# Optimization experiments

Hardware: AMD Instinct MI355X
Metric: run time of the kernel (lower is better)

The kernel has to match this reference:

```python
import jax, jax.numpy as jnp
import numpy as np

B, S, D = 128, 256, 768          # batch, seq (pre-sentinel), encoder dim
ARC, TAG = 500, 100              # arc / tag representation dims
LAYERS, TOPK = 2, 8              # config['gnn_layers'], config['top_k']
SP = S + 1                       # seq_len after head sentinel


def setup_inputs() -> dict:
    key = jax.random.key(0)
    ks = jax.random.split(key, 32)
    sc = 0.02
    inp = {
        'inputs': jax.random.normal(ks[0], (B, S, D), jnp.float32),
        'tag_embeddings': jax.random.randint(ks[1], (B, S), 0, 50),
        'mask': jnp.ones((B, S), jnp.int32),
        'head_indices': jax.random.randint(ks[2], (B, S), 0, S),
        'head_tags': jax.random.randint(ks[3], (B, S), 0, 50),
        # parameters
        'head_sentinel': jax.random.normal(ks[4], (D,), jnp.float32),
        'W_ha': jax.random.normal(ks[5], (D, ARC)) * sc, 'b_ha': jnp.zeros((ARC,)),
        'W_da': jax.random.normal(ks[6], (D, ARC)) * sc, 'b_da': jnp.zeros((ARC,)),
        'W_ht': jax.random.normal(ks[7], (D, TAG)) * sc, 'b_ht': jnp.zeros((TAG,)),
        'W_dt': jax.random.normal(ks[8], (D, TAG)) * sc, 'b_dt': jnp.zeros((TAG,)),
        # bilinear attention: use_input_biases=True -> (ARC+1, ARC+1), plus scalar bias
        'bil_W': jax.random.normal(ks[9], (LAYERS + 1, ARC + 1, ARC + 1)) * sc,
        'bil_b': jnp.zeros((LAYERS + 1,)),
        # GCNConv params (PyG: x @ W, symmetric-normalized aggregate, + bias)
        'c1a_W': jax.random.normal(ks[10], (ARC, ARC)) * sc, 'c1a_b': jnp.zeros((ARC,)),
        'c2a_W': jax.random.normal(ks[11], (ARC, ARC)) * sc, 'c2a_b': jnp.zeros((ARC,)),
        'c1r_W': jax.random.normal(ks[12], (TAG, TAG)) * sc, 'c1r_b': jnp.zeros((TAG,)),
        'c2r_W': jax.random.normal(ks[13], (TAG, TAG)) * sc, 'c2r_b': jnp.zeros((TAG,)),
    }
    return inp


def bilinear_attn(m1, m2, W, b):
    # AllenNLP BilinearMatrixAttention with use_input_biases=True
    ones1 = jnp.ones(m1.shape[:-1] + (1,), m1.dtype)
    m1b = jnp.concatenate([m1, ones1], -1)
    m2b = jnp.concatenate([m2, ones1], -1)
    return jnp.einsum('bie,ef,bjf->bij', m1b, W, m2b) + b


def batch_top_k(probs, k):
    # probs: [B, SP, SP] row-softmaxed; edge j(head)->i(dep) for each row's top-k cols,
    # with global (batched) node indexing.
    vals, idx = jax.lax.top_k(probs, k)                      # [B, SP, k]
    offs = (jnp.arange(B) * SP)[:, None, None]
    src = (idx + offs).reshape(-1)
    dst = (jnp.broadcast_to(jnp.arange(SP)[None, :, None], idx.shape) + offs).reshape(-1)
    return src, dst, vals.reshape(-1)


def gcn_conv(x, src, dst, ew, W, b):
    # PyG GCNConv: x@W, add self-loops (weight 1), sym norm, scatter-add at dst, + bias
    N = x.shape[0]
    x = x @ W
    loop = jnp.arange(N)
    row = jnp.concatenate([src, loop])
    col = jnp.concatenate([dst, loop])
    w = jnp.concatenate([ew, jnp.ones((N,), x.dtype)])
    deg = jax.ops.segment_sum(w, col, num_segments=N)
    dinv = jnp.where(deg > 0, jax.lax.rsqrt(deg), 0.0)
    norm = dinv[row] * w * dinv[col]
    out = jax.ops.segment_sum(x[row] * norm[:, None], col, num_segments=N)
    return out + b


def reference(inputs, tag_embeddings, mask, head_indices, head_tags,
              head_sentinel, W_ha, b_ha, W_da, b_da, W_ht, b_ht, W_dt, b_dt,
              bil_W, bil_b, c1a_W, c1a_b, c2a_W, c2a_b, c1r_W, c1r_b, c2r_W, c2r_b):
    elu = jax.nn.elu
    x = jnp.concatenate([jnp.broadcast_to(head_sentinel, (B, 1, D)), inputs], axis=1)  # [B,SP,D]
    head_arc = elu(x @ W_ha + b_ha)
    dept_arc = elu(x @ W_da + b_da)
    head_tag = elu(x @ W_ht + b_ht)
    dep_tag = elu(x @ W_dt + b_dt)

    def two_conv(feat, W1, b1, W2, b2, src, dst, ew):
        h = gcn_conv(feat.reshape(B * SP, -1), src, dst, ew, W1, b1)
        h = gcn_conv(elu(h), src, dst, ew, W2, b2)
        return h.reshape(B, SP, -1)

    for k in range(LAYERS):
        arc_logits = bilinear_attn(head_arc, dept_arc, bil_W[k], bil_b[k])
        arc_probs = jax.nn.softmax(arc_logits, axis=-1)
        src, dst, ew = batch_top_k(arc_probs, TOPK)
        head_arc = two_conv(head_arc, c1a_W, c1a_b, c2a_W, c2a_b, src, dst, ew)
        dept_arc = two_conv(dept_arc, c1a_W, c1a_b, c2a_W, c2a_b, src, dst, ew)
        head_tag = two_conv(head_tag, c1r_W, c1r_b, c2r_W, c2r_b, src, dst, ew)
        dep_tag = two_conv(dep_tag, c1r_W, c1r_b, c2r_W, c2r_b, src, dst, ew)

    arc_logits = bilinear_attn(head_arc, dept_arc, bil_W[-1], bil_b[-1])
    return arc_logits, head_tag, dep_tag
```

## Files before the change

kernel.cpp:

```cpp
#include <hip/hip_runtime.h>
#include <hip/hip_bf16.h>
#include <math.h>
#include <cstddef>

namespace {

constexpr int kB   = 128;
constexpr int kS   = 256;
constexpr int kD   = 768;
constexpr int kSP  = 257;
constexpr int kN   = kB * kSP;
constexpr int kARC = 500;
constexpr int kTAG = 100;
constexpr int KA   = 512;
constexpr int KT   = 128;

typedef __attribute__((ext_vector_type(8))) short short8;
typedef __attribute__((ext_vector_type(4))) float floatx4;
typedef __attribute__((ext_vector_type(2))) float floatx2;
typedef __attribute__((ext_vector_type(4))) unsigned short ushort4v;
typedef __attribute__((ext_vector_type(2))) unsigned short ushort2v;
typedef __hip_bfloat16 bf;

__device__ __forceinline__ float bfval(bf h) { return __bfloat162float(h); }
__device__ __forceinline__ unsigned short bfbits(bf h) {
  unsigned short u; __builtin_memcpy(&u, &h, 2); return u;
}
__device__ __forceinline__ void splitf(float x, bf* h, bf* l) {
  bf hh = __float2bfloat16(x);
  *h = hh;
  *l = __float2bfloat16(x - __bfloat162float(hh));
}

__device__ __forceinline__ void gload16(const bf* g, bf* l) {
  __builtin_amdgcn_global_load_lds(
      (const __attribute__((address_space(1))) void*)g,
      (__attribute__((address_space(3))) void*)l, 16, 0, 0);
}

__global__ void detect_dtype_n(const unsigned* __restrict__ raw, int* __restrict__ flag,
                               int nwords) {
  int lane = threadIdx.x;
  int ok = 0, nz = 0;
  if (lane < nwords) {
    unsigned w = raw[lane];
    if (w != 0u) {
      nz = 1;
      int e = (w >> 7) & 0xFF;
      ok = (e >= 90 && e <= 140);
    }
  }
  unsigned long long ball_ok = __ballot(ok);
  unsigned long long ball_nz = __ballot(nz);
  if (lane == 0) {
    int cok = __popcll(ball_ok), cnz = __popcll(ball_nz);
    flag[0] = (cok * 4 >= cnz * 3) ? 1 : 0;
  }
}

__device__ __forceinline__ float rawload(const void* p, size_t i, int bfm) {
  return bfm ? __bfloat162float(((const bf*)p)[i]) : ((const float*)p)[i];
}

__global__ void conv_off(const void* __restrict__ src, float* __restrict__ dst,
                         int n, long off, const int* __restrict__ flag) {
  int i = blockIdx.x * 256 + threadIdx.x;
  if (i >= n) return;
  dst[i] = rawload(src, (size_t)off + i, *flag);
}

__global__ void wsplit_t(const void* __restrict__ src, const int* __restrict__ flag,
                         long srcOff, int ldsrc, int K, int N, int Kpad,
                         bf* __restrict__ Wh, bf* __restrict__ Wl) {
  long idx = (long)blockIdx.x * 256 + threadIdx.x;
  if (idx >= (long)N * Kpad) return;
  int n = (int)(idx / Kpad), k = (int)(idx % Kpad);
  float v = (k < K) ? rawload(src, (size_t)srcOff + (size_t)k * ldsrc + n, *flag) : 0.f;
  bf h, l;
  splitf(v, &h, &l);
  Wh[idx] = h; Wl[idx] = l;
}

__global__ void xsplit(const void* __restrict__ inp, const void* __restrict__ sent,
                       const int* __restrict__ fi, const int* __restrict__ fs,
                       bf* __restrict__ xh, bf* __restrict__ xl, int g0, int NG) {
  long idx = (long)blockIdx.x * 256 + threadIdx.x;
  long tot = (long)NG * (kD / 4);
  if (idx >= tot) return;
  int n = (int)(idx / (kD / 4));
  int k = (int)(idx % (kD / 4)) * 4;
  int b = n / kSP, r = n - b * kSP;
  const void* src;
  size_t base;
  int bfm;
  if (r == 0) { src = sent; base = (size_t)k; bfm = *fs; }
  else {
    src = inp;
    base = ((size_t)((g0 + b) * kS + (r - 1))) * kD + k;
    bfm = *fi;
  }
  float v[4];
  if (bfm) {
    ushort4v s = *(const ushort4v*)((const unsigned short*)src + base);
#pragma unroll
    for (int j = 0; j < 4; ++j) {
      bf h; unsigned short u = s[j];
      __builtin_memcpy(&h, &u, 2);
      v[j] = __bfloat162float(h);
    }
  } else {
    floatx4 f4 = *(const floatx4*)((const float*)src + base);
#pragma unroll
    for (int j = 0; j < 4; ++j) v[j] = f4[j];
  }
  ushort4v h4, l4;
#pragma unroll
  for (int j = 0; j < 4; ++j) {
    bf h, l;
    splitf(v[j], &h, &l);
    h4[j] = bfbits(h); l4[j] = bfbits(l);
  }
  size_t o = (size_t)n * kD + k;
  *(ushort4v*)((unsigned short*)xh + o) = h4;
  *(ushort4v*)((unsigned short*)xl + o) = l4;
}

constexpr int BM = 128, BN = 128, BK = 32;

template <int EPI, int OUTF32>
__global__ __launch_bounds__(256) void gemm_sp(
    const bf* __restrict__ Ah, const bf* __restrict__ Al, int lda,
    const bf* __restrict__ Bh, const bf* __restrict__ Bl, int ldb,
    bf* __restrict__ Ch, bf* __restrict__ Cl, float* __restrict__ Cf, int ldc,
    int M, int N, int K, const float* __restrict__ bias) {
  __shared__ bf sAh[2][BM][BK];
  __shared__ bf sAl[2][BM][BK];
  __shared__ bf sBh[2][BN][BK];
  __shared__ bf sBl[2][BN][BK];
  const int tid = threadIdx.x;
  const int lane = tid & 63, wave = tid >> 6;
  const int quad = lane >> 4, l15 = lane & 15;
  const int wm = (wave >> 1) * 64, wn = (wave & 1) * 64;
  const int m0 = blockIdx.x * BM, n0 = blockIdx.y * BN;
  const int lrow = lane >> 2, lkof = (lane & 3) * 8;

  const bf *pAh[2], *pAl[2], *pBh[2], *pBl[2];
  int rb[2];
#pragma unroll
  for (int jj = 0; jj < 2; ++jj) {
    rb[jj] = wave * 32 + jj * 16;
    int gm = m0 + rb[jj] + lrow; if (gm > M - 1) gm = M - 1;
    int gn = n0 + rb[jj] + lrow; if (gn > N - 1) gn = N - 1;
    pAh[jj] = Ah + (size_t)gm * lda + lkof;
    pAl[jj] = Al + (size_t)gm * lda + lkof;
    pBh[jj] = Bh + (size_t)gn * ldb + lkof;
    pBl[jj] = Bl + (size_t)gn * ldb + lkof;
  }

  auto stage = [&](int bi, int k0) {
#pragma unroll
    for (int jj = 0; jj < 2; ++jj) {
      gload16(pAh[jj] + k0, &sAh[bi][rb[jj]][0]);
      gload16(pAl[jj] + k0, &sAl[bi][rb[jj]][0]);
      gload16(pBh[jj] + k0, &sBh[bi][rb[jj]][0]);
      gload16(pBl[jj] + k0, &sBl[bi][rb[jj]][0]);
    }
  };

  floatx4 acc[4][4] = {};
  stage(0, 0);
  int cur = 0;
  for (int k0 = 0; k0 < K; k0 += BK) {
    __syncthreads();
    if (k0 + BK < K) stage(cur ^ 1, k0 + BK);
    short8 a_h[4], a_l[4], b_h[4], b_l[4];
#pragma unroll
    for (int t = 0; t < 4; ++t) {
      a_h[t] = *(const short8*)&sAh[cur][wm + t * 16 + l15][quad * 8];
      a_l[t] = *(const short8*)&sAl[cur][wm + t * 16 + l15][quad * 8];
      b_h[t] = *(const short8*)&sBh[cur][wn + t * 16 + l15][quad * 8];
      b_l[t] = *(const short8*)&sBl[cur][wn + t * 16 + l15][quad * 8];
    }
#pragma unroll
    for (int mt = 0; mt < 4; ++mt)
#pragma unroll
      for (int nt = 0; nt < 4; ++nt) {
        acc[mt][nt] = __builtin_amdgcn_mfma_f32_16x16x32_bf16(a_h[mt], b_h[nt], acc[mt][nt], 0, 0, 0);
        acc[mt][nt] = __builtin_amdgcn_mfma_f32_16x16x32_bf16(a_h[mt], b_l[nt], acc[mt][nt], 0, 0, 0);
        acc[mt][nt] = __builtin_amdgcn_mfma_f32_16x16x32_bf16(a_l[mt], b_h[nt], acc[mt][nt], 0, 0, 0);
      }
    cur ^= 1;
  }
#pragma unroll
  for (int mt = 0; mt < 4; ++mt)
#pragma unroll
    for (int reg = 0; reg < 4; ++reg) {
      int m = m0 + wm + mt * 16 + quad * 4 + reg;
      if (m >= M) continue;
#pragma unroll
      for (int nt = 0; nt < 4; ++nt) {
        int n = n0 + wn + nt * 16 + l15;
        if (OUTF32) {
          if (n < N) {
            float v = acc[mt][nt][reg];
            if (EPI >= 1) v += bias[n];
            if (EPI == 1) v = v > 0.f ? v : expm1f(v);
            Cf[(size_t)m * ldc + n] = v;
          }
        } else {
          size_t o = (size_t)m * ldc + n;
          if (n < N) {
            float v = acc[mt][nt][reg];
            if (EPI >= 1) v += bias[n];
            if (EPI == 1) v = v > 0.f ? v : expm1f(v);
            bf h, l;
            splitf(v, &h, &l);
            Ch[o] = h; Cl[o] = l;
          } else if (n < ldc) {
            Ch[o] = __float2bfloat16(0.f);
            Cl[o] = __float2bfloat16(0.f);
          }
        }
      }
    }
}

__global__ __launch_bounds__(256) void bilnt_sp(
    const bf* __restrict__ Th, const bf* __restrict__ Tl,
    const bf* __restrict__ Fh, const bf* __restrict__ Fl,
    float* __restrict__ out, const float* __restrict__ bilb, int bidx,
    int g0, int globOut) {
  __shared__ bf sAh[2][BM][BK];
  __shared__ bf sAl[2][BM][BK];
  __shared__ bf sBh[2][BN][BK];
  __shared__ bf sBl[2][BN][BK];
  const int z = blockIdx.z;
  const int tid = threadIdx.x;
  const int lane = tid & 63, wave = tid >> 6;
  const int quad = lane >> 4, l15 = lane & 15;
  const int wm = (wave >> 1) * 64, wn = (wave & 1) * 64;
  const int m0 = blockIdx.x * BM, n0 = blockIdx.y * BN;
  const int lrow = lane >> 2, lkof = (lane & 3) * 8;
  const bf* Ah = Th + (size_t)z * kSP * KA;
  const bf* Al = Tl + (size_t)z * kSP * KA;
  const bf* Bh = Fh + (size_t)z * kSP * KA;
  const bf* Bl = Fl + (size_t)z * kSP * KA;

  const bf *pAh[2], *pAl[2], *pBh[2], *pBl[2];
  int rb[2];
#pragma unroll
  for (int jj = 0; jj < 2; ++jj) {
    rb[jj] = wave * 32 + jj * 16;
    int gm = m0 + rb[jj] + lrow; if (gm > kSP - 1) gm = kSP - 1;
    int gn = n0 + rb[jj] + lrow; if (gn > kSP - 1) gn = kSP - 1;
    pAh[jj] = Ah + (size_t)gm * KA + lkof;
    pAl[jj] = Al + (size_t)gm * KA + lkof;
    pBh[jj] = Bh + (size_t)gn * KA + lkof;
    pBl[jj] = Bl + (size_t)gn * KA + lkof;
  }

  auto stage = [&](int bi, int k0) {
#pragma unroll
    for (int jj = 0; jj < 2; ++jj) {
      gload16(pAh[jj] + k0, &sAh[bi][rb[jj]][0]);
      gload16(pAl[jj] + k0, &sAl[bi][rb[jj]][0]);
      gload16(pBh[jj] + k0, &sBh[bi][rb[jj]][0]);
      gload16(pBl[jj] + k0, &sBl[bi][rb[jj]][0]);
    }
  };

  floatx4 acc[4][4] = {};
  stage(0, 0);
  int cur = 0;
  for (int k0 = 0; k0 < KA; k0 += BK) {
    __syncthreads();
    if (k0 + BK < KA) stage(cur ^ 1, k0 + BK);
    short8 a_h[4], a_l[4], b_h[4], b_l[4];
#pragma unroll
    for (int t = 0; t < 4; ++t) {
      a_h[t] = *(const short8*)&sAh[cur][wm + t * 16 + l15][quad * 8];
      a_l[t] = *(const short8*)&sAl[cur][wm + t * 16 + l15][quad * 8];
      b_h[t] = *(const short8*)&sBh[cur][wn + t * 16 + l15][quad * 8];
      b_l[t] = *(const short8*)&sBl[cur][wn + t * 16 + l15][quad * 8];
    }
#pragma unroll
    for (int mt = 0; mt < 4; ++mt)
#pragma unroll
      for (int nt = 0; nt < 4; ++nt) {
        acc[mt][nt] = __builtin_amdgcn_mfma_f32_16x16x32_bf16(a_h[mt], b_h[nt], acc[mt][nt], 0, 0, 0);
        acc[mt][nt] = __builtin_amdgcn_mfma_f32_16x16x32_bf16(a_h[mt], b_l[nt], acc[mt][nt], 0, 0, 0);
        acc[mt][nt] = __builtin_amdgcn_mfma_f32_16x16x32_bf16(a_l[mt], b_h[nt], acc[mt][nt], 0, 0, 0);
      }
    cur ^= 1;
  }
  const float sb = bilb[bidx];
  const int bb = globOut ? (g0 + z) : z;
#pragma unroll
  for (int mt = 0; mt < 4; ++mt)
#pragma unroll
    for (int reg = 0; reg < 4; ++reg) {
      int i = m0 + wm + mt * 16 + quad * 4 + reg;
      if (i >= kSP) continue;
      float rowterm = bfval(Ah[(size_t)i * KA + 500]) + bfval(Al[(size_t)i * KA + 500]) + sb;
#pragma unroll
      for (int nt = 0; nt < 4; ++nt) {
        int j = n0 + wn + nt * 16 + l15;
        if (j >= kSP) continue;
        out[((size_t)bb * kSP + i) * kSP + j] = acc[mt][nt][reg] + rowterm;
      }
    }
}

__global__ void softmax_topk(const float* __restrict__ logits,
                             int* __restrict__ idx8,
                             float* __restrict__ val8,
                             float* __restrict__ dinv) {
  const int row = blockIdx.x;
  const int lane = threadIdx.x;
  const int rowbase = row - (row % kSP);
  const float* L = logits + (size_t)row * kSP;
  float v[5];
  int c[5];
#pragma unroll
  for (int q = 0; q < 5; ++q) {
    int j = lane + q * 64;
    c[q] = j;
    v[q] = (j < kSP) ? L[j] : -INFINITY;
  }
  float m = v[0];
#pragma unroll
  for (int q = 1; q < 5; ++q) m = fmaxf(m, v[q]);
  for (int off = 32; off > 0; off >>= 1) m = fmaxf(m, __shfl_xor(m, off));
  float s = 0.f;
#pragma unroll
  for (int q = 0; q < 5; ++q) s += expf(v[q] - m);
  for (int off = 32; off > 0; off >>= 1) s += __shfl_xor(s, off);
  const float invs = 1.f / s;
  float degsum = 0.f;
  for (int t = 0; t < 8; ++t) {
    float bvv = -INFINITY;
    int bii = kSP;
#pragma unroll
    for (int q = 0; q < 5; ++q)
      if (v[q] > bvv) { bvv = v[q]; bii = c[q]; }
    for (int off = 32; off > 0; off >>= 1) {
      float ov = __shfl_xor(bvv, off);
      int oi = __shfl_xor(bii, off);
      if (ov > bvv || (ov == bvv && oi < bii)) { bvv = ov; bii = oi; }
    }
    float p = expf(bvv - m) * invs;
    degsum += p;
    if (lane == 0) { idx8[row * 8 + t] = rowbase + bii; val8[row * 8 + t] = p; }
#pragma unroll
    for (int q = 0; q < 5; ++q)
      if (c[q] == bii) v[q] = -INFINITY;
  }
  if (lane == 0) dinv[row] = 1.f / sqrtf(1.f + degsum);
}

template <int ELU, int OUTF32>
__global__ void gcn_agg(const float* __restrict__ Y, int ldy, int F,
                        const int* __restrict__ idx8, const float* __restrict__ val8,
                        const float* __restrict__ dinv, const float* __restrict__ bias,
                        bf* __restrict__ Zh, bf* __restrict__ Zl,
                        float* __restrict__ Zf, int ldzf) {
  const int n = blockIdx.x;
  __shared__ float w[9];
  __shared__ int srcs[8];
  const int t = threadIdx.x;
  if (t < 8) {
    int s = idx8[n * 8 + t];
    srcs[t] = s;
    w[t] = dinv[n] * val8[n * 8 + t] * dinv[s];
  } else if (t == 8) {
    float di = dinv[n];
    w[8] = di * di;
  }
  __syncthreads();
  const int lim = OUTF32 ? F : ldy;
  for (int f = t * 2; f < lim; f += (int)blockDim.x * 2) {
    size_t on = (size_t)n * ldy + f;
    if (!OUTF32 && f >= F) {
      ushort2v zz = {0, 0};
      *(ushort2v*)((unsigned short*)Zh + on) = zz;
      *(ushort2v*)((unsigned short*)Zl + on) = zz;
      continue;
    }
    floatx2 y0 = *(const floatx2*)(Y + on);
    float a0 = w[8] * y0[0], a1 = w[8] * y0[1];
#pragma unroll
    for (int e = 0; e < 8; ++e) {
      floatx2 ys = *(const floatx2*)(Y + (size_t)srcs[e] * ldy + f);
      a0 += w[e] * ys[0];
      a1 += w[e] * ys[1];
    }
    a0 += bias[f];
    a1 += bias[f + 1];
    if (ELU) {
      a0 = a0 > 0.f ? a0 : expm1f(a0);
      a1 = a1 > 0.f ? a1 : expm1f(a1);
    }
    if (OUTF32) {
      floatx2 o = {a0, a1};
      *(floatx2*)(Zf + (size_t)n * ldzf + f) = o;
    } else {
      bf h0, l0, h1, l1;
      splitf(a0, &h0, &l0);
      splitf(a1, &h1, &l1);
      ushort2v hv = {bfbits(h0), bfbits(h1)};
      ushort2v lv = {bfbits(l0), bfbits(l1)};
      *(ushort2v*)((unsigned short*)Zh + on) = hv;
      *(ushort2v*)((unsigned short*)Zl + on) = lv;
    }
  }
}

}

extern "C" void kernel_launch(void* const* d_in, const int* in_sizes, int n_in,
                              void* d_out, int out_size, void* d_ws, size_t ws_size,
                              hipStream_t stream) {
  (void)out_size;

  const int roleSize[20] = {kB * kS * kD, kD,
                            kD * kARC, kARC, kD * kARC, kARC,
                            kD * kTAG, kTAG, kD * kTAG, kTAG,
                            3 * 501 * 501, 3,
                            kARC * kARC, kARC, kARC * kARC, kARC,
                            kTAG * kTAG, kTAG, kTAG * kTAG, kTAG};
  const int roleOcc[20]  = {0, 0, 0, 0, 1, 1, 0, 0, 1, 1, 0, 0,
                            0, 2, 1, 3, 0, 2, 1, 3};
  int roleIdx[20] = {0, 5, 6, 7, 8, 9, 10, 11, 12, 13, 14, 15,
                     16, 17, 18, 19, 20, 21, 22, 23};
  for (int r = 0; r < 20; ++r) {
    int occ = 0, found = -1;
    for (int i = 0; i < n_in; ++i) {
      if (in_sizes[i] == roleSize[r]) {
        if (occ == roleOcc[r]) { found = i; break; }
        ++occ;
      }
    }
    if (found >= 0) roleIdx[r] = found;
    else if (roleIdx[r] >= n_in) roleIdx[r] = 0;
  }
  const void* src_of[20];
  for (int r = 0; r < 20; ++r) src_of[r] = d_in[roleIdx[r]];

  auto need_bytes = [](int GB) -> size_t {
    size_t NG = (size_t)GB * kSP, s = 0;
    auto al = [&](size_t b) { s += (b + 255) & ~(size_t)255; };
    al(256);
    for (int i = 0; i < 4; ++i) al((size_t)kARC * kD * 2);
    for (int i = 0; i < 4; ++i) al((size_t)kTAG * kD * 2);
    al(kARC * 4); al(kARC * 4); al(kTAG * 4); al(kTAG * 4);
    for (int i = 0; i < 6; ++i) al((size_t)501 * KA * 2);
    al(3 * 501 * 4); al(256);
    for (int i = 0; i < 4; ++i) al((size_t)kARC * KA * 2);
    for (int i = 0; i < 4; ++i) al((size_t)kTAG * KT * 2);
    al(kARC * 4); al(kARC * 4); al(kTAG * 4); al(kTAG * 4);
    al(NG * kD * 2); al(NG * kD * 2);
    for (int i = 0; i < 4; ++i) al(NG * KA * 2);
    for (int i = 0; i < 4; ++i) al(NG * KT * 2);
    al(NG * KA * 2); al(NG * KA * 2);
    al(NG * KA * 4);
    al(NG * kSP * 4);
    al(NG * 8 * 4); al(NG * 8 * 4); al(NG * 4);
    return s;
  };
  int GB = 1;
  for (int cand : {128, 64, 32, 16, 8, 4, 2, 1})
    if (need_bytes(cand) <= ws_size) { GB = cand; break; }
  const int G = kB / GB;
  const int NG = GB * kSP;
  const int mb = (NG + BM - 1) / BM;

  char* ws = (char*)d_ws;
  size_t off = 0;
  auto alloc = [&](size_t bytes) -> void* {
    void* p = ws + off;
    off += (bytes + 255) & ~(size_t)255;
    return p;
  };
  int* flags = (int*)alloc(256);
  bf *WtHAh = (bf*)alloc((size_t)kARC * kD * 2), *WtHAl = (bf*)alloc((size_t)kARC * kD * 2);
  bf *WtDAh = (bf*)alloc((size_t)kARC * kD * 2), *WtDAl = (bf*)alloc((size_t)kARC * kD * 2);
  bf *WtHTh = (bf*)alloc((size_t)kTAG * kD * 2), *WtHTl = (bf*)alloc((size_t)kTAG * kD * 2);
  bf *WtDTh = (bf*)alloc((size_t)kTAG * kD * 2), *WtDTl = (bf*)alloc((size_t)kTAG * kD * 2);
  float* bha = (float*)alloc(kARC * 4);
  float* bda = (float*)alloc(kARC * 4);
  float* bht = (float*)alloc(kTAG * 4);
  float* bdt = (float*)alloc(kTAG * 4);
  bf* bilWh[3]; bf* bilWl[3];
  for (int k = 0; k < 3; ++k) {
    bilWh[k] = (bf*)alloc((size_t)501 * KA * 2);
    bilWl[k] = (bf*)alloc((size_t)501 * KA * 2);
  }
  float* brow = (float*)alloc(3 * 501 * 4);
  float* bilbf = (float*)alloc(256);
  bf *c1ah = (bf*)alloc((size_t)kARC * KA * 2), *c1al = (bf*)alloc((size_t)kARC * KA * 2);
  bf *c2ah = (bf*)alloc((size_t)kARC * KA * 2), *c2al = (bf*)alloc((size_t)kARC * KA * 2);
  bf *c1rh = (bf*)alloc((size_t)kTAG * KT * 2), *c1rl = (bf*)alloc((size_t)kTAG * KT * 2);
  bf *c2rh = (bf*)alloc((size_t)kTAG * KT * 2), *c2rl = (bf*)alloc((size_t)kTAG * KT * 2);
  float* c1ab = (float*)alloc(kARC * 4);
  float* c2ab = (float*)alloc(kARC * 4);
  float* c1rb = (float*)alloc(kTAG * 4);
  float* c2rb = (float*)alloc(kTAG * 4);
  bf *xh = (bf*)alloc((size_t)NG * kD * 2), *xl = (bf*)alloc((size_t)NG * kD * 2);
  bf *fHAh = (bf*)alloc((size_t)NG * KA * 2), *fHAl = (bf*)alloc((size_t)NG * KA * 2);
  bf *fDAh = (bf*)alloc((size_t)NG * KA * 2), *fDAl = (bf*)alloc((size_t)NG * KA * 2);
  bf *fHTh = (bf*)alloc((size_t)NG * KT * 2), *fHTl = (bf*)alloc((size_t)NG * KT * 2);
  bf *fDTh = (bf*)alloc((size_t)NG * KT * 2), *fDTl = (bf*)alloc((size_t)NG * KT * 2);
  bf *Yh = (bf*)alloc((size_t)NG * KA * 2), *Yl = (bf*)alloc((size_t)NG * KA * 2);
  float* Yf = (float*)alloc((size_t)NG * KA * 4);
  float* logits = (float*)alloc((size_t)NG * kSP * 4);
  int*   idx8 = (int*)alloc((size_t)NG * 8 * 4);
  float* val8 = (float*)alloc((size_t)NG * 8 * 4);
  float* dinv = (float*)alloc((size_t)NG * 4);

  for (int r = 0; r < 20; ++r) {
    int n = roleSize[r];
    int nwords = n / 4; if (nwords < 1) nwords = 1; if (nwords > 64) nwords = 64;
    detect_dtype_n<<<1, 64, 0, stream>>>((const unsigned*)src_of[r], flags + r, nwords);
  }
  auto cvt = [&](int role, float* dst, int n, long o) {
    conv_off<<<(n + 255) / 256, 256, 0, stream>>>(src_of[role], dst, n, o, flags + role);
  };
  cvt(3, bha, kARC, 0); cvt(5, bda, kARC, 0); cvt(7, bht, kTAG, 0); cvt(9, bdt, kTAG, 0);
  cvt(11, bilbf, 3, 0);
  cvt(13, c1ab, kARC, 0); cvt(15, c2ab, kARC, 0); cvt(17, c1rb, kTAG, 0); cvt(19, c2rb, kTAG, 0);
  auto wsp = [&](int role, long o, int ldsrc, int K, int N, int Kpad, bf* Wh, bf* Wl) {
    long tot = (long)N * Kpad;
    wsplit_t<<<(int)((tot + 255) / 256), 256, 0, stream>>>(src_of[role], flags + role, o,
                                                           ldsrc, K, N, Kpad, Wh, Wl);
  };
  wsp(2, 0, kARC, kD, kARC, kD, WtHAh, WtHAl);
  wsp(4, 0, kARC, kD, kARC, kD, WtDAh, WtDAl);
  wsp(6, 0, kTAG, kD, kTAG, kD, WtHTh, WtHTl);
  wsp(8, 0, kTAG, kD, kTAG, kD, WtDTh, WtDTl);
  for (int k = 0; k < 3; ++k) {
    wsp(10, (long)k * 501 * 501, 501, 500, 501, KA, bilWh[k], bilWl[k]);
    cvt(10, brow + k * 501, 501, (long)k * 501 * 501 + 500 * 501);
  }
  wsp(12, 0, kARC, kARC, kARC, KA, c1ah, c1al);
  wsp(14, 0, kARC, kARC, kARC, KA, c2ah, c2al);
  wsp(16, 0, kTAG, kTAG, kTAG, KT, c1rh, c1rl);
  wsp(18, 0, kTAG, kTAG, kTAG, KT, c2rh, c2rl);

  float* outp = (float*)d_out;
  const size_t arc_elems = (size_t)kB * kSP * kSP;

  for (int g = 0; g < G; ++g) {
    const int g0 = g * GB;

    {
      long tot = (long)NG * (kD / 4);
      xsplit<<<(int)((tot + 255) / 256), 256, 0, stream>>>(
          src_of[0], src_of[1], flags + 0, flags + 1, xh, xl, g0, NG);
    }
    gemm_sp<1, 0><<<dim3(mb, 4), 256, 0, stream>>>(xh, xl, kD, WtHAh, WtHAl, kD,
                                                   fHAh, fHAl, nullptr, KA, NG, kARC, kD, bha);
    gemm_sp<1, 0><<<dim3(mb, 4), 256, 0, stream>>>(xh, xl, kD, WtDAh, WtDAl, kD,
                                                   fDAh, fDAl, nullptr, KA, NG, kARC, kD, bda);
    gemm_sp<1, 0><<<dim3(mb, 1), 256, 0, stream>>>(xh, xl, kD, WtHTh, WtHTl, kD,
                                                   fHTh, fHTl, nullptr, KT, NG, kTAG, kD, bht);
    gemm_sp<1, 0><<<dim3(mb, 1), 256, 0, stream>>>(xh, xl, kD, WtDTh, WtDTl, kD,
                                                   fDTh, fDTl, nullptr, KT, NG, kTAG, kD, bdt);

    for (int k = 0; k < 2; ++k) {
      gemm_sp<2, 0><<<dim3(mb, 4), 256, 0, stream>>>(fHAh, fHAl, KA, bilWh[k], bilWl[k], KA,
                                                     Yh, Yl, nullptr, KA, NG, 501, KA,
                                                     brow + k * 501);
      bilnt_sp<<<dim3(3, 3, GB), 256, 0, stream>>>(Yh, Yl, fDAh, fDAl, logits, bilbf, k, g0, 0);
      softmax_topk<<<NG, 64, 0, stream>>>(logits, idx8, val8, dinv);

      bf* fh[2] = {fHAh, fDAh};
      bf* fl[2] = {fHAl, fDAl};
      for (int ff = 0; ff < 2; ++ff) {
        gemm_sp<0, 1><<<dim3(mb, 4), 256, 0, stream>>>(fh[ff], fl[ff], KA, c1ah, c1al, KA,
                                                       nullptr, nullptr, Yf, KA, NG, kARC, KA,
                                                       nullptr);
        gcn_agg<1, 0><<<NG, 256, 0, stream>>>(Yf, KA, kARC, idx8, val8, dinv, c1ab,
                                              Yh, Yl, nullptr, 0);
        gemm_sp<0, 1><<<dim3(mb, 4), 256, 0, stream>>>(Yh, Yl, KA, c2ah, c2al, KA,
                                                       nullptr, nullptr, Yf, KA, NG, kARC, KA,
                                                       nullptr);
        gcn_agg<0, 0><<<NG, 256, 0, stream>>>(Yf, KA, kARC, idx8, val8, dinv, c2ab,
                                              fh[ff], fl[ff], nullptr, 0);
      }
      bf* th[2] = {fHTh, fDTh};
      bf* tl[2] = {fHTl, fDTl};
      for (int ff = 0; ff < 2; ++ff) {
        gemm_sp<0, 1><<<dim3(mb, 1), 256, 0, stream>>>(th[ff], tl[ff], KT, c1rh, c1rl, KT,
                                                       nullptr, nullptr, Yf, KT, NG, kTAG, KT,
                                                       nullptr);
        gcn_agg<1, 0><<<NG, 64, 0, stream>>>(Yf, KT, kTAG, idx8, val8, dinv, c1rb,
                                             Yh, Yl, nullptr, 0);
        gemm_sp<0, 1><<<dim3(mb, 1), 256, 0, stream>>>(Yh, Yl, KT, c2rh, c2rl, KT,
                                                       nullptr, nullptr, Yf, KT, NG, kTAG, KT,
                                                       nullptr);
        if (k == 1) {
          float* dst = outp + arc_elems + (ff == 1 ? (size_t)kN * kTAG : 0)
                       + (size_t)g0 * kSP * kTAG;
          gcn_agg<0, 1><<<NG, 64, 0, stream>>>(Yf, KT, kTAG, idx8, val8, dinv, c2rb,
                                               nullptr, nullptr, dst, kTAG);
        } else {
          gcn_agg<0, 0><<<NG, 64, 0, stream>>>(Yf, KT, kTAG, idx8, val8, dinv, c2rb,
                                               th[ff], tl[ff], nullptr, 0);
        }
      }
    }

    gemm_sp<2, 0><<<dim3(mb, 4), 256, 0, stream>>>(fHAh, fHAl, KA, bilWh[2], bilWl[2], KA,
                                                   Yh, Yl, nullptr, KA, NG, 501, KA,
                                                   brow + 2 * 501);
    bilnt_sp<<<dim3(3, 3, GB), 256, 0, stream>>>(Yh, Yl, fDAh, fDAl, outp, bilbf, 2, g0, 1);
  }
}
```

Measured before the change: 3.395 ms.

## Interleave head/dep features and batch projection, GCN GEMMs and aggregation across both

Concatenates the head and dependent projection weights so each input projection runs as one wider GEMM into an interleaved feature buffer (head/dep side by side per row). The GCN convolutions then treat head and dep rows as a 2*NG-row matrix, so the two per-feature launches become one GEMM and one aggregation kernel each, with aggregation remapping source indices to the interleaved layout. It also adds an XCD-aware block swizzle to the GEMM, bilinear and aggregation kernels to improve L2 locality. The aim is fewer launches and larger, better-occupied GEMMs, at the cost of wider padded buffers, extra zero-fill kernels and more workspace.

```diff
diff --git a/kernel.cpp b/kernel.cpp
--- a/kernel.cpp
+++ b/kernel.cpp
@@ -14,6 +14,8 @@
 constexpr int kTAG = 100;
 constexpr int KA   = 512;
 constexpr int KT   = 128;
+constexpr int NPA  = 1024;
+constexpr int NPT  = 256;
 
 typedef __attribute__((ext_vector_type(8))) short short8;
 typedef __attribute__((ext_vector_type(4))) float floatx4;
@@ -32,10 +34,21 @@
   *l = __float2bfloat16(x - __bfloat162float(hh));
 }
 
+__device__ __forceinline__ int swz8(int lid, int total) {
+  int q = total >> 3, r = total & 7;
+  int c = lid & 7, p = lid >> 3;
+  return (c < r ? c * (q + 1) : r * (q + 1) + (c - r) * q) + p;
+}
+
 __device__ __forceinline__ void gload16(const bf* g, bf* l) {
   __builtin_amdgcn_global_load_lds(
       (const __attribute__((address_space(1))) void*)g,
       (__attribute__((address_space(3))) void*)l, 16, 0, 0);
+}
+
+__global__ void zerofill(unsigned* __restrict__ p, long n4) {
+  long i = (long)blockIdx.x * 256 + threadIdx.x;
+  if (i < n4) p[i] = 0u;
 }
 
 __global__ void detect_dtype_n(const unsigned* __restrict__ raw, int* __restrict__ flag,
@@ -141,7 +154,9 @@
   const int lane = tid & 63, wave = tid >> 6;
   const int quad = lane >> 4, l15 = lane & 15;
   const int wm = (wave >> 1) * 64, wn = (wave & 1) * 64;
-  const int m0 = blockIdx.x * BM, n0 = blockIdx.y * BN;
+  const int gy = gridDim.y;
+  const int sw = swz8(blockIdx.x + blockIdx.y * gridDim.x, gridDim.x * gy);
+  const int m0 = (sw / gy) * BM, n0 = (sw % gy) * BN;
   const int lrow = lane >> 2, lkof = (lane & 3) * 8;
 
   const bf *pAh[2], *pAl[2], *pBh[2], *pBl[2];
@@ -227,24 +242,27 @@
 
 __global__ __launch_bounds__(256) void bilnt_sp(
     const bf* __restrict__ Th, const bf* __restrict__ Tl,
-    const bf* __restrict__ Fh, const bf* __restrict__ Fl,
+    const bf* __restrict__ Fh, const bf* __restrict__ Fl, int ldf,
     float* __restrict__ out, const float* __restrict__ bilb, int bidx,
     int g0, int globOut) {
   __shared__ bf sAh[2][BM][BK];
   __shared__ bf sAl[2][BM][BK];
   __shared__ bf sBh[2][BN][BK];
   __shared__ bf sBl[2][BN][BK];
-  const int z = blockIdx.z;
   const int tid = threadIdx.x;
   const int lane = tid & 63, wave = tid >> 6;
   const int quad = lane >> 4, l15 = lane & 15;
   const int wm = (wave >> 1) * 64, wn = (wave & 1) * 64;
-  const int m0 = blockIdx.x * BM, n0 = blockIdx.y * BN;
+  const int gx = gridDim.x, gxy = gridDim.x * gridDim.y;
+  const int sw = swz8(blockIdx.x + gx * blockIdx.y + gxy * blockIdx.z, gxy * gridDim.z);
+  const int z = sw / gxy;
+  const int rem = sw % gxy;
+  const int m0 = (rem % gx) * BM, n0 = (rem / gx) * BN;
   const int lrow = lane >> 2, lkof = (lane & 3) * 8;
   const bf* Ah = Th + (size_t)z * kSP * KA;
   const bf* Al = Tl + (size_t)z * kSP * KA;
-  const bf* Bh = Fh + (size_t)z * kSP * KA;
-  const bf* Bl = Fl + (size_t)z * kSP * KA;
+  const bf* Bh = Fh + (size_t)z * kSP * ldf;
+  const bf* Bl = Fl + (size_t)z * kSP * ldf;
 
   const bf *pAh[2], *pAl[2], *pBh[2], *pBl[2];
   int rb[2];
@@ -255,8 +273,8 @@
     int gn = n0 + rb[jj] + lrow; if (gn > kSP - 1) gn = kSP - 1;
     pAh[jj] = Ah + (size_t)gm * KA + lkof;
     pAl[jj] = Al + (size_t)gm * KA + lkof;
-    pBh[jj] = Bh + (size_t)gn * KA + lkof;
-    pBl[jj] = Bl + (size_t)gn * KA + lkof;
+    pBh[jj] = Bh + (size_t)gn * ldf + lkof;
+    pBl[jj] = Bl + (size_t)gn * ldf + lkof;
   }
 
   auto stage = [&](int bi, int k0) {
@@ -363,23 +381,24 @@
                         const int* __restrict__ idx8, const float* __restrict__ val8,
                         const float* __restrict__ dinv, const float* __restrict__ bias,
                         bf* __restrict__ Zh, bf* __restrict__ Zl,
-                        float* __restrict__ Zf, int ldzf) {
-  const int n = blockIdx.x;
+                        float* __restrict__ Zf, int ldzf, long halfStr) {
+  const int r = swz8(blockIdx.x, gridDim.x);
+  const int m = r >> 1, p = r & 1;
   __shared__ float w[9];
   __shared__ int srcs[8];
   const int t = threadIdx.x;
   if (t < 8) {
-    int s = idx8[n * 8 + t];
-    srcs[t] = s;
-    w[t] = dinv[n] * val8[n * 8 + t] * dinv[s];
+    int s = idx8[m * 8 + t];
+    srcs[t] = 2 * s + p;
+    w[t] = dinv[m] * val8[m * 8 + t] * dinv[s];
   } else if (t == 8) {
-    float di = dinv[n];
+    float di = dinv[m];
     w[8] = di * di;
   }
   __syncthreads();
   const int lim = OUTF32 ? F : ldy;
   for (int f = t * 2; f < lim; f += (int)blockDim.x * 2) {
-    size_t on = (size_t)n * ldy + f;
+    size_t on = (size_t)r * ldy + f;
     if (!OUTF32 && f >= F) {
       ushort2v zz = {0, 0};
       *(ushort2v*)((unsigned short*)Zh + on) = zz;
@@ -401,8 +420,9 @@
       a1 = a1 > 0.f ? a1 : expm1f(a1);
     }
     if (OUTF32) {
+      float* zp = Zf + (size_t)p * halfStr + (size_t)m * ldzf + f;
       floatx2 o = {a0, a1};
-      *(floatx2*)(Zf + (size_t)n * ldzf + f) = o;
+      *(floatx2*)zp = o;
     } else {
       bf h0, l0, h1, l1;
       splitf(a0, &h0, &l0);
@@ -450,19 +470,20 @@
     size_t NG = (size_t)GB * kSP, s = 0;
     auto al = [&](size_t b) { s += (b + 255) & ~(size_t)255; };
     al(256);
-    for (int i = 0; i < 4; ++i) al((size_t)kARC * kD * 2);
-    for (int i = 0; i < 4; ++i) al((size_t)kTAG * kD * 2);
-    al(kARC * 4); al(kARC * 4); al(kTAG * 4); al(kTAG * 4);
+    al((size_t)NPA * kD * 2); al((size_t)NPA * kD * 2);
+    al((size_t)NPT * kD * 2); al((size_t)NPT * kD * 2);
+    al(NPA * 4); al(NPT * 4);
     for (int i = 0; i < 6; ++i) al((size_t)501 * KA * 2);
     al(3 * 501 * 4); al(256);
     for (int i = 0; i < 4; ++i) al((size_t)kARC * KA * 2);
     for (int i = 0; i < 4; ++i) al((size_t)kTAG * KT * 2);
     al(kARC * 4); al(kARC * 4); al(kTAG * 4); al(kTAG * 4);
     al(NG * kD * 2); al(NG * kD * 2);
-    for (int i = 0; i < 4; ++i) al(NG * KA * 2);
-    for (int i = 0; i < 4; ++i) al(NG * KT * 2);
+    al(NG * NPA * 2); al(NG * NPA * 2);
+    al(NG * NPT * 2); al(NG * NPT * 2);
     al(NG * KA * 2); al(NG * KA * 2);
-    al(NG * KA * 4);
+    al(NG * NPA * 2); al(NG * NPA * 2);
+    al(NG * NPA * 4);
     al(NG * kSP * 4);
     al(NG * 8 * 4); al(NG * 8 * 4); al(NG * 4);
     return s;
@@ -472,7 +493,8 @@
     if (need_bytes(cand) <= ws_size) { GB = cand; break; }
   const int G = kB / GB;
   const int NG = GB * kSP;
-  const int mb = (NG + BM - 1) / BM;
+  const int mb  = (NG + BM - 1) / BM;
+  const int mb2 = (2 * NG + BM - 1) / BM;
 
   char* ws = (char*)d_ws;
   size_t off = 0;
@@ -482,14 +504,10 @@
     return p;
   };
   int* flags = (int*)alloc(256);
-  bf *WtHAh = (bf*)alloc((size_t)kARC * kD * 2), *WtHAl = (bf*)alloc((size_t)kARC * kD * 2);
-  bf *WtDAh = (bf*)alloc((size_t)kARC * kD * 2), *WtDAl = (bf*)alloc((size_t)kARC * kD * 2);
-  bf *WtHTh = (bf*)alloc((size_t)kTAG * kD * 2), *WtHTl = (bf*)alloc((size_t)kTAG * kD * 2);
-  bf *WtDTh = (bf*)alloc((size_t)kTAG * kD * 2), *WtDTl = (bf*)alloc((size_t)kTAG * kD * 2);
-  float* bha = (float*)alloc(kARC * 4);
-  float* bda = (float*)alloc(kARC * 4);
-  float* bht = (float*)alloc(kTAG * 4);
-  float* bdt = (float*)alloc(kTAG * 4);
+  bf *WtABh = (bf*)alloc((size_t)NPA * kD * 2), *WtABl = (bf*)alloc((size_t)NPA * kD * 2);
+  bf *WtTBh = (bf*)alloc((size_t)NPT * kD * 2), *WtTBl = (bf*)alloc((size_t)NPT * kD * 2);
+  float* bpa = (float*)alloc(NPA * 4);
+  float* bpt = (float*)alloc(NPT * 4);
   bf* bilWh[3]; bf* bilWl[3];
   for (int k = 0; k < 3; ++k) {
     bilWh[k] = (bf*)alloc((size_t)501 * KA * 2);
@@ -506,12 +524,11 @@
   float* c1rb = (float*)alloc(kTAG * 4);
   float* c2rb = (float*)alloc(kTAG * 4);
   bf *xh = (bf*)alloc((size_t)NG * kD * 2), *xl = (bf*)alloc((size_t)NG * kD * 2);
-  bf *fHAh = (bf*)alloc((size_t)NG * KA * 2), *fHAl = (bf*)alloc((size_t)NG * KA * 2);
-  bf *fDAh = (bf*)alloc((size_t)NG * KA * 2), *fDAl = (bf*)alloc((size_t)NG * KA * 2);
-  bf *fHTh = (bf*)alloc((size_t)NG * KT * 2), *fHTl = (bf*)alloc((size_t)NG * KT * 2);
-  bf *fDTh = (bf*)alloc((size_t)NG * KT * 2), *fDTl = (bf*)alloc((size_t)NG * KT * 2);
-  bf *Yh = (bf*)alloc((size_t)NG * KA * 2), *Yl = (bf*)alloc((size_t)NG * KA * 2);
-  float* Yf = (float*)alloc((size_t)NG * KA * 4);
+  bf *FAh = (bf*)alloc((size_t)NG * NPA * 2), *FAl = (bf*)alloc((size_t)NG * NPA * 2);
+  bf *FTh = (bf*)alloc((size_t)NG * NPT * 2), *FTl = (bf*)alloc((size_t)NG * NPT * 2);
+  bf *Th = (bf*)alloc((size_t)NG * KA * 2), *Tl = (bf*)alloc((size_t)NG * KA * 2);
+  bf *Z2h = (bf*)alloc((size_t)NG * NPA * 2), *Z2l = (bf*)alloc((size_t)NG * NPA * 2);
+  float* Yf = (float*)alloc((size_t)NG * NPA * 4);
   float* logits = (float*)alloc((size_t)NG * kSP * 4);
   int*   idx8 = (int*)alloc((size_t)NG * 8 * 4);
   float* val8 = (float*)alloc((size_t)NG * 8 * 4);
@@ -525,18 +542,27 @@
   auto cvt = [&](int role, float* dst, int n, long o) {
     conv_off<<<(n + 255) / 256, 256, 0, stream>>>(src_of[role], dst, n, o, flags + role);
   };
-  cvt(3, bha, kARC, 0); cvt(5, bda, kARC, 0); cvt(7, bht, kTAG, 0); cvt(9, bdt, kTAG, 0);
-  cvt(11, bilbf, 3, 0);
-  cvt(13, c1ab, kARC, 0); cvt(15, c2ab, kARC, 0); cvt(17, c1rb, kTAG, 0); cvt(19, c2rb, kTAG, 0);
   auto wsp = [&](int role, long o, int ldsrc, int K, int N, int Kpad, bf* Wh, bf* Wl) {
     long tot = (long)N * Kpad;
     wsplit_t<<<(int)((tot + 255) / 256), 256, 0, stream>>>(src_of[role], flags + role, o,
                                                            ldsrc, K, N, Kpad, Wh, Wl);
   };
-  wsp(2, 0, kARC, kD, kARC, kD, WtHAh, WtHAl);
-  wsp(4, 0, kARC, kD, kARC, kD, WtDAh, WtDAl);
-  wsp(6, 0, kTAG, kD, kTAG, kD, WtHTh, WtHTl);
-  wsp(8, 0, kTAG, kD, kTAG, kD, WtDTh, WtDTl);
+  auto zf = [&](void* p, size_t bytes) {
+    long n4 = (long)(bytes / 4);
+    zerofill<<<(int)((n4 + 255) / 256), 256, 0, stream>>>((unsigned*)p, n4);
+  };
+
+  zf(WtABh, (size_t)NPA * kD * 2); zf(WtABl, (size_t)NPA * kD * 2);
+  zf(WtTBh, (size_t)NPT * kD * 2); zf(WtTBl, (size_t)NPT * kD * 2);
+  zf(bpa, NPA * 4); zf(bpt, NPT * 4);
+  wsp(2, 0, kARC, kD, kARC, kD, WtABh, WtABl);
+  wsp(4, 0, kARC, kD, kARC, kD, WtABh + (size_t)KA * kD, WtABl + (size_t)KA * kD);
+  wsp(6, 0, kTAG, kD, kTAG, kD, WtTBh, WtTBl);
+  wsp(8, 0, kTAG, kD, kTAG, kD, WtTBh + (size_t)KT * kD, WtTBl + (size_t)KT * kD);
+  cvt(3, bpa, kARC, 0); cvt(5, bpa + KA, kARC, 0);
+  cvt(7, bpt, kTAG, 0); cvt(9, bpt + KT, kTAG, 0);
+  cvt(11, bilbf, 3, 0);
+  cvt(13, c1ab, kARC, 0); cvt(15, c2ab, kARC, 0); cvt(17, c1rb, kTAG, 0); cvt(19, c2rb, kTAG, 0);
   for (int k = 0; k < 3; ++k) {
     wsp(10, (long)k * 501 * 501, 501, 500, 501, KA, bilWh[k], bilWl[k]);
     cvt(10, brow + k * 501, 501, (long)k * 501 * 501 + 500 * 501);
@@ -557,62 +583,49 @@
       xsplit<<<(int)((tot + 255) / 256), 256, 0, stream>>>(
           src_of[0], src_of[1], flags + 0, flags + 1, xh, xl, g0, NG);
     }
-    gemm_sp<1, 0><<<dim3(mb, 4), 256, 0, stream>>>(xh, xl, kD, WtHAh, WtHAl, kD,
-                                                   fHAh, fHAl, nullptr, KA, NG, kARC, kD, bha);
-    gemm_sp<1, 0><<<dim3(mb, 4), 256, 0, stream>>>(xh, xl, kD, WtDAh, WtDAl, kD,
-                                                   fDAh, fDAl, nullptr, KA, NG, kARC, kD, bda);
-    gemm_sp<1, 0><<<dim3(mb, 1), 256, 0, stream>>>(xh, xl, kD, WtHTh, WtHTl, kD,
-                                                   fHTh, fHTl, nullptr, KT, NG, kTAG, kD, bht);
-    gemm_sp<1, 0><<<dim3(mb, 1), 256, 0, stream>>>(xh, xl, kD, WtDTh, WtDTl, kD,
-                                                   fDTh, fDTl, nullptr, KT, NG, kTAG, kD, bdt);
+    gemm_sp<1, 0><<<dim3(mb, NPA / BN), 256, 0, stream>>>(
+        xh, xl, kD, WtABh, WtABl, kD, FAh, FAl, nullptr, NPA, NG, NPA, kD, bpa);
+    gemm_sp<1, 0><<<dim3(mb, NPT / BN), 256, 0, stream>>>(
+        xh, xl, kD, WtTBh, WtTBl, kD, FTh, FTl, nullptr, NPT, NG, NPT, kD, bpt);
 
     for (int k = 0; k < 2; ++k) {
-      gemm_sp<2, 0><<<dim3(mb, 4), 256, 0, stream>>>(fHAh, fHAl, KA, bilWh[k], bilWl[k], KA,
-                                                     Yh, Yl, nullptr, KA, NG, 501, KA,
-                                                     brow + k * 501);
-      bilnt_sp<<<dim3(3, 3, GB), 256, 0, stream>>>(Yh, Yl, fDAh, fDAl, logits, bilbf, k, g0, 0);
+      gemm_sp<2, 0><<<dim3(mb, 4), 256, 0, stream>>>(
+          FAh, FAl, NPA, bilWh[k], bilWl[k], KA, Th, Tl, nullptr, KA, NG, 501, KA,
+          brow + k * 501);
+      bilnt_sp<<<dim3(3, 3, GB), 256, 0, stream>>>(
+          Th, Tl, FAh + KA, FAl + KA, NPA, logits, bilbf, k, g0, 0);
       softmax_topk<<<NG, 64, 0, stream>>>(logits, idx8, val8, dinv);
 
-      bf* fh[2] = {fHAh, fDAh};
-      bf* fl[2] = {fHAl, fDAl};
-      for (int ff = 0; ff < 2; ++ff) {
-        gemm_sp<0, 1><<<dim3(mb, 4), 256, 0, stream>>>(fh[ff], fl[ff], KA, c1ah, c1al, KA,
-                                                       nullptr, nullptr, Yf, KA, NG, kARC, KA,
-                                                       nullptr);
-        gcn_agg<1, 0><<<NG, 256, 0, stream>>>(Yf, KA, kARC, idx8, val8, dinv, c1ab,
-                                              Yh, Yl, nullptr, 0);
-        gemm_sp<0, 1><<<dim3(mb, 4), 256, 0, stream>>>(Yh, Yl, KA, c2ah, c2al, KA,
-                                                       nullptr, nullptr, Yf, KA, NG, kARC, KA,
-                                                       nullptr);
-        gcn_agg<0, 0><<<NG, 256, 0, stream>>>(Yf, KA, kARC, idx8, val8, dinv, c2ab,
-                                              fh[ff], fl[ff], nullptr, 0);
+      gemm_sp<0, 1><<<dim3(mb2, 4), 256, 0, stream>>>(
+          FAh, FAl, KA, c1ah, c1al, KA, nullptr, nullptr, Yf, KA, 2 * NG, kARC, KA, nullptr);
+      gcn_agg<1, 0><<<2 * NG, 256, 0, stream>>>(Yf, KA, kARC, idx8, val8, dinv, c1ab,
+                                                Z2h, Z2l, nullptr, 0, 0);
+      gemm_sp<0, 1><<<dim3(mb2, 4), 256, 0, stream>>>(
+          Z2h, Z2l, KA, c2ah, c2al, KA, nullptr, nullptr, Yf, KA, 2 * NG, kARC, KA, nullptr);
+      gcn_agg<0, 0><<<2 * NG, 256, 0, stream>>>(Yf, KA, kARC, idx8, val8, dinv, c2ab,
+                                                FAh, FAl, nullptr, 0, 0);
+
+      gemm_sp<0, 1><<<dim3(mb2, 1), 256, 0, stream>>>(
+          FTh, FTl, KT, c1rh, c1rl, KT, nullptr, nullptr, Yf, KT, 2 * NG, kTAG, KT, nullptr);
+      gcn_agg<1, 0><<<2 * NG, 64, 0, stream>>>(Yf, KT, kTAG, idx8, val8, dinv, c1rb,
+                                               Z2h, Z2l, nullptr, 0, 0);
+      gemm_sp<0, 1><<<dim3(mb2, 1), 256, 0, stream>>>(
+          Z2h, Z2l, KT, c2rh, c2rl, KT, nullptr, nullptr, Yf, KT, 2 * NG, kTAG, KT, nullptr);
+      if (k == 1) {
+        float* dst = outp + arc_elems + (size_t)g0 * kSP * kTAG;
+        gcn_agg<0, 1><<<2 * NG, 64, 0, stream>>>(Yf, KT, kTAG, idx8, val8, dinv, c2rb,
+                                                 nullptr, nullptr, dst, kTAG,
+                                                 (long)kN * kTAG);
+      } else {
+        gcn_agg<0, 0><<<2 * NG, 64, 0, stream>>>(Yf, KT, kTAG, idx8, val8, dinv, c2rb,
+                                                 FTh, FTl, nullptr, 0, 0);
       }
-      bf* th[2] = {fHTh, fDTh};
-      bf* tl[2] = {fHTl, fDTl};
-      for (int ff = 0; ff < 2; ++ff) {
-        gemm_sp<0, 1><<<dim3(mb, 1), 256, 0, stream>>>(th[ff], tl[ff], KT, c1rh, c1rl, KT,
-                                                       nullptr, nullptr, Yf, KT, NG, kTAG, KT,
-                                                       nullptr);
-        gcn_agg<1, 0><<<NG, 64, 0, stream>>>(Yf, KT, kTAG, idx8, val8, dinv, c1rb,
-                                             Yh, Yl, nullptr, 0);
-        gemm_sp<0, 1><<<dim3(mb, 1), 256, 0, stream>>>(Yh, Yl, KT, c2rh, c2rl, KT,
-                                                       nullptr, nullptr, Yf, KT, NG, kTAG, KT,
-                                                       nullptr);
-        if (k == 1) {
-          float* dst = outp + arc_elems + (ff == 1 ? (size_t)kN * kTAG : 0)
-                       + (size_t)g0 * kSP * kTAG;
-          gcn_agg<0, 1><<<NG, 64, 0, stream>>>(Yf, KT, kTAG, idx8, val8, dinv, c2rb,
-                                               nullptr, nullptr, dst, kTAG);
-        } else {
-          gcn_agg<0, 0><<<NG, 64, 0, stream>>>(Yf, KT, kTAG, idx8, val8, dinv, c2rb,
-                                               th[ff], tl[ff], nullptr, 0);
-        }
-      }
-    }
-
-    gemm_sp<2, 0><<<dim3(mb, 4), 256, 0, stream>>>(fHAh, fHAl, KA, bilWh[2], bilWl[2], KA,
-                                                   Yh, Yl, nullptr, KA, NG, 501, KA,
-                                                   brow + 2 * 501);
-    bilnt_sp<<<dim3(3, 3, GB), 256, 0, stream>>>(Yh, Yl, fDAh, fDAl, outp, bilbf, 2, g0, 1);
-  }
-}
+    }
+
+    gemm_sp<2, 0><<<dim3(mb, 4), 256, 0, stream>>>(
+        FAh, FAl, NPA, bilWh[2], bilWl[2], KA, Th, Tl, nullptr, KA, NG, 501, KA,
+        brow + 2 * 501);
+    bilnt_sp<<<dim3(3, 3, GB), 256, 0, stream>>>(
+        Th, Tl, FAh + KA, FAl + KA, NPA, outp, bilbf, 2, g0, 1);
+  }
+}
```

Result: faster. 2.798 ms (-17.6%).
